# Kernel tuning notes

Hardware: AMD Instinct MI355X
Metric: run time of the kernel (lower is better)

The kernel has to match this reference:

```python
import jax, jax.numpy as jnp
import numpy as np

D_MODEL = 1024
NUM_HEADS = 16
SEQ_LEN = 2048
BATCH = 2
THETA = 10000.0


def apply_rope(x, positions, theta):
    # x: [..., seq, d_k]; positions: [seq]
    dk = x.shape[-1]
    half = dk // 2
    k = jnp.arange(half, dtype=jnp.float32)
    inv_freq = theta ** (-2.0 * k / dk)                 # [half]
    ang = positions.astype(jnp.float32)[:, None] * inv_freq  # [seq, half]
    cos, sin = jnp.cos(ang), jnp.sin(ang)
    xe = x[..., 0::2]   # even members of adjacent pairs
    xo = x[..., 1::2]
    out_e = cos * xe - sin * xo
    out_o = sin * xe + cos * xo
    # interleave pairs back: [..., seq, half, 2] -> [..., seq, dk]
    return jnp.stack([out_e, out_o], axis=-1).reshape(x.shape)


def setup_inputs() -> dict:
    key = jax.random.key(0)
    kx, kq, kk, kv, ko = jax.random.split(key, 5)
    sig = 1.0 / np.sqrt(D_MODEL)
    def tn(k):
        return jnp.clip(jax.random.normal(k, (D_MODEL, D_MODEL), jnp.float32), -3.0, 3.0) * sig
    return {
        "x": jax.random.normal(kx, (BATCH, SEQ_LEN, D_MODEL), jnp.float32),
        "q_proj_weight": tn(kq),
        "k_proj_weight": tn(kk),
        "v_proj_weight": tn(kv),
        "o_proj_weight": tn(ko),
        "token_positions": jnp.arange(SEQ_LEN, dtype=jnp.int32),
    }


def reference(x, q_proj_weight, k_proj_weight, v_proj_weight, o_proj_weight, token_positions):
    h = NUM_HEADS
    d = x.shape[-1]
    dh = d // h
    seq = x.shape[-2]
    Wq = q_proj_weight.reshape(h, dh, d)
    Wk = k_proj_weight.reshape(h, dh, d)
    Wv = v_proj_weight.reshape(h, dh, d)
    Q = jnp.einsum('bsd,hed->bhse', x, Wq)
    K = jnp.einsum('bsd,hed->bhse', x, Wk)
    V = jnp.einsum('bsd,hed->bhse', x, Wv)
    Q = apply_rope(Q, token_positions, THETA)
    K = apply_rope(K, token_positions, THETA)
    scores = jnp.einsum('bhqe,bhke->bhqk', Q, K) / jnp.sqrt(jnp.float32(dh))
    mask = jnp.tril(jnp.ones((seq, seq), dtype=bool))
    scores = jnp.where(mask, scores, -jnp.inf)
    probs = jax.nn.softmax(scores, axis=-1)
    att = jnp.einsum('bhqk,bhke->bhqe', probs, V)       # [b, h, s, dh]
    att = att.transpose(0, 2, 1, 3).reshape(x.shape[0], seq, d)  # concat heads
    return jnp.einsum('bsh,dh->bsd', att, o_proj_weight)
```

## Files before the change

### kernel.cpp

```cpp
#include <hip/hip_runtime.h>
#include <hip/hip_bf16.h>
#include <cstdint>
#include <cstddef>

#define DEV static __device__ __forceinline__

typedef __bf16 bf16x8 __attribute__((ext_vector_type(8)));
typedef float f32x4 __attribute__((ext_vector_type(4)));
typedef unsigned short u16;

static constexpr int BATCH = 2, SEQ = 2048, DM = 1024, NH = 16, DH = 64;
static constexpr int Kdim = 1024;
static constexpr int BS = BATCH * SEQ;

DEV u16 f2b(float f) {
  uint32_t u = __builtin_bit_cast(uint32_t, f);
  u += 0x7FFFu + ((u >> 16) & 1u);
  return (u16)(u >> 16);
}

DEV void gload_lds16(const void* g, void* l) {
  __builtin_amdgcn_global_load_lds((const __attribute__((address_space(1))) void*)g,
                                   (__attribute__((address_space(3))) void*)l, 16, 0, 0);
}

DEV void plswap32(uint32_t& a, uint32_t& b) {
  asm("v_permlane32_swap_b32 %0, %1" : "+v"(a), "+v"(b));
}
DEV void plswap16(uint32_t& a, uint32_t& b) {
  asm("v_permlane16_swap_b32 %0, %1" : "+v"(a), "+v"(b));
}

__global__ __launch_bounds__(256) void cast_all(const float* __restrict__ x,
    const float* __restrict__ wq, const float* __restrict__ wk,
    const float* __restrict__ wv, const float* __restrict__ wo,
    const int* __restrict__ pos,
    u16* __restrict__ xb, u16* __restrict__ wqb, u16* __restrict__ wkb,
    u16* __restrict__ wvb, u16* __restrict__ wob, float2* __restrict__ tab) {
  const int NX = (BATCH * SEQ * DM) / 4;
  const int NW = (DM * DM) / 4;
  const int NT = SEQ * 32;
  int i = blockIdx.x * blockDim.x + threadIdx.x;
  const int stride = gridDim.x * blockDim.x;
  for (; i < NX + 4 * NW + NT; i += stride) {
    if (i < NX + 4 * NW) {
      const float* src; u16* dst; int off;
      if (i < NX) { src = x; dst = xb; off = i; }
      else {
        const int j = i - NX, seg = j >> 18;
        off = j & (NW - 1);
        src = seg == 0 ? wq : seg == 1 ? wk : seg == 2 ? wv : wo;
        dst = seg == 0 ? wqb : seg == 1 ? wkb : seg == 2 ? wvb : wob;
      }
      float4 v = ((const float4*)src)[off];
      ushort4 o;
      o.x = f2b(v.x); o.y = f2b(v.y); o.z = f2b(v.z); o.w = f2b(v.w);
      ((ushort4*)dst)[off] = o;
    } else {
      const int t = i - NX - 4 * NW;
      const int s = t >> 5, j = t & 31;
      const float ang = (float)pos[s] * exp2f((float)j * -0.4152410118609203f);
      float sn, cs;
      sincosf(ang, &sn, &cs);
      tab[t] = make_float2(cs, sn);
    }
  }
}

template <int BN, bool OUTF32, int ROPE>
DEV void gemm_core(const u16* __restrict__ A, const u16* __restrict__ Bm,
                   void* __restrict__ Cout, int ldC, int m0, int n0,
                   u16* __restrict__ As, u16* __restrict__ Bs,
                   const float2* __restrict__ tab) {
  const int tid = threadIdx.x;
  const int lane = tid & 63, wid = tid >> 6;
  const int wr = (wid >> 1) * 64, wc = (wid & 1) * (BN / 2);
  const int frow = lane & 15, fgrp = lane >> 4;
  constexpr int NF = BN / 32;
  constexpr int BSZ = BN * 32;
  constexpr int NK = Kdim / 32;
  f32x4 acc[4][NF] = {};

  const int c0 = tid, c1 = tid + 256;
  const int ra0 = c0 >> 2, sa0 = (c0 & 3) ^ ((ra0 >> 1) & 3);
  const int ra1 = c1 >> 2, sa1 = (c1 & 3) ^ ((ra1 >> 1) & 3);
  const size_t gA0 = (size_t)(m0 + ra0) * Kdim + sa0 * 8;
  const size_t gA1 = (size_t)(m0 + ra1) * Kdim + sa1 * 8;
  const size_t gB0 = (size_t)(n0 + ra0) * Kdim + sa0 * 8;
  const size_t gB1 = (size_t)(n0 + ra1) * Kdim + sa1 * 8;

#define GSTAGE(bufi, kofs)                                                      \
  do {                                                                          \
    gload_lds16(A + gA0 + (kofs), As + (bufi) * 4096 + wid * 512);              \
    gload_lds16(A + gA1 + (kofs), As + (bufi) * 4096 + wid * 512 + 2048);       \
    gload_lds16(Bm + gB0 + (kofs), Bs + (bufi) * BSZ + wid * 512);              \
    if (BN == 128)                                                              \
      gload_lds16(Bm + gB1 + (kofs), Bs + (bufi) * BSZ + wid * 512 + 2048);     \
  } while (0)

  GSTAGE(0, 0);
  for (int kt = 0; kt < NK; ++kt) {
    const int buf = kt & 1;
    if (kt + 1 < NK) {
      GSTAGE((kt + 1) & 1, (kt + 1) * 32);
      if (BN == 128) asm volatile("s_waitcnt vmcnt(4)" ::: "memory");
      else           asm volatile("s_waitcnt vmcnt(3)" ::: "memory");
    } else {
      asm volatile("s_waitcnt vmcnt(0)" ::: "memory");
    }
    __builtin_amdgcn_s_barrier();

    bf16x8 af[4], bfr[NF];
#pragma unroll
    for (int i = 0; i < 4; ++i) {
      const int ra = wr + i * 16 + frow;
      af[i] = *(const bf16x8*)((const char*)(As + buf * 4096) + ra * 64 +
                               ((fgrp ^ ((ra >> 1) & 3)) * 16));
    }
#pragma unroll
    for (int f = 0; f < NF; ++f) {
      const int rb = wc + f * 16 + frow;
      bfr[f] = *(const bf16x8*)((const char*)(Bs + buf * BSZ) + rb * 64 +
                                ((fgrp ^ ((rb >> 1) & 3)) * 16));
    }
#pragma unroll
    for (int mi = 0; mi < 4; ++mi)
#pragma unroll
      for (int f = 0; f < NF; ++f)
        acc[mi][f] = __builtin_amdgcn_mfma_f32_16x16x32_bf16(af[mi], bfr[f], acc[mi][f], 0, 0, 0);

    __builtin_amdgcn_s_barrier();
  }
#undef GSTAGE

  const int colb = n0 + wc + frow;
  const int rowb = m0 + wr + fgrp * 4;
  if (ROPE) {
#pragma unroll
    for (int mi = 0; mi < 4; ++mi)
#pragma unroll
      for (int f = 0; f < NF; ++f) {
        const int col = colb + f * 16;
        const int j = (col & 63) >> 1;
#pragma unroll
        for (int r = 0; r < 4; ++r) {
          const float v = acc[mi][f][r];
          const float partner = __shfl_xor(v, 1);
          const int row = rowb + mi * 16 + r;
          const float2 cs_ = tab[(row & (SEQ - 1)) * 32 + j];
          float outv = (col & 1) ? fmaf(cs_.y, partner, cs_.x * v)
                                 : fmaf(cs_.x, v, -cs_.y * partner);
          if (ROPE == 1) outv *= 0.18033688011112043f;
          acc[mi][f][r] = outv;
        }
      }
  }
#pragma unroll
  for (int mi = 0; mi < 4; ++mi)
#pragma unroll
    for (int f = 0; f < NF; ++f)
#pragma unroll
      for (int r = 0; r < 4; ++r) {
        const int row = rowb + mi * 16 + r;
        const int col = colb + f * 16;
        const float v = acc[mi][f][r];
        if (OUTF32) ((float*)Cout)[(size_t)row * ldC + col] = v;
        else        ((u16*)Cout)[(size_t)row * ldC + col] = f2b(v);
      }
}

__global__ __launch_bounds__(256) void gemm_qkvt(const u16* __restrict__ xb,
    const u16* __restrict__ wq, const u16* __restrict__ wk, const u16* __restrict__ wv,
    u16* __restrict__ Qb, u16* __restrict__ Kb, u16* __restrict__ Vtb,
    const float2* __restrict__ tab) {
  __shared__ u16 As[2][4096], Bs[2][2048];
  const int f = blockIdx.x, z = blockIdx.z;
  const int xcd = f & 7, j = f >> 3;
  if (z == 0) {
    const int m0 = (xcd * 4 + (j >> 4)) * 128, n0 = (j & 15) * 64;
    gemm_core<64, false, 1>(xb, wq, Qb, DM, m0, n0, &As[0][0], &Bs[0][0], tab);
  } else if (z == 1) {
    const int m0 = (xcd * 4 + (j >> 4)) * 128, n0 = (j & 15) * 64;
    gemm_core<64, false, 2>(xb, wk, Kb, DM, m0, n0, &As[0][0], &Bs[0][0], tab);
  } else {
    const int m0 = xcd * 128, n0 = j * 64;
    gemm_core<64, false, 0>(wv, xb, Vtb, BS, m0, n0, &As[0][0], &Bs[0][0], nullptr);
  }
}

__global__ __launch_bounds__(256) void gemm_o(const u16* __restrict__ attb,
                                              const u16* __restrict__ wob,
                                              float* __restrict__ out) {
  __shared__ u16 As[2][4096], Bs[2][2048];
  const int f = blockIdx.x;
  const int xcd = f & 7, k = f >> 3;
  const int grp = xcd * 8 + (k >> 3);
  const int m0 = (grp >> 1) * 128;
  const int n0 = ((grp & 1) * 8 + (k & 7)) * 64;
  gemm_core<64, true, 0>(attb, wob, out, DM, m0, n0, &As[0][0], &Bs[0][0], nullptr);
}

__global__ __launch_bounds__(512, 4) void attn_kernel(const u16* __restrict__ Qb,
                                                      const u16* __restrict__ Kb,
                                                      const u16* __restrict__ Vtb,
                                                      u16* __restrict__ attb) {
  __shared__ __align__(16) unsigned char SM[73728];
  float* Of = (float*)SM;
  float* Ld = (float*)(SM + 65536);

  const int tid = threadIdx.x, lane = tid & 63, wid = tid >> 6;
  const int qh = wid >> 2, kq = wid & 3;
  const int flat = (int)blockIdx.x + 16 * (int)blockIdx.y;
  const int orig = (flat & 7) * 64 + (flat >> 3);
  const int xq = orig & 15;
  const int bh = orig >> 4;
  const int b = bh >> 4, h = bh & 15;
  const size_t base_bh = ((size_t)b * SEQ) * DM + h * DH;
  const int frow = lane & 15, fgrp = lane >> 4;
  const int kq32 = kq * 32;
  const int swz = (frow & 7) << 4;

  const u16* Ksrcs[2];
  const u16* Vsrcs[2];
#pragma unroll
  for (int i = 0; i < 2; ++i) {
    const int c = tid + i * 512;
    const int rk = c >> 3, s8 = (c & 7) ^ (rk & 7);
    Ksrcs[i] = Kb + base_bh + (size_t)rk * DM + s8 * 8;
    const int rv = c >> 4, s16 = (c & 15) ^ (rv & 7);
    Vsrcs[i] = Vtb + (size_t)(h * DH + rv) * BS + (size_t)b * SEQ + s16 * 8;
  }
  const int rq = tid >> 3, sq = (tid & 7) ^ (rq & 7);

#pragma unroll 1
  for (int phase = 0; phase < 2; ++phase) {
    const int qt = phase ? xq : 31 - xq;
    const int q0 = qt * 64;
    const int nkv = (qt >> 1) + 1;

    gload_lds16(Qb + base_bh + (size_t)(q0 + rq) * DM + sq * 8, (char*)SM + 65536 + tid * 16);
#pragma unroll
    for (int i = 0; i < 2; ++i) {
      gload_lds16(Ksrcs[i], (char*)SM + i * 8192 + tid * 16);
      gload_lds16(Vsrcs[i], (char*)SM + 32768 + i * 8192 + tid * 16);
    }
    __syncthreads();

    bf16x8 qf[2][2];
#pragma unroll
    for (int qs = 0; qs < 2; ++qs)
#pragma unroll
      for (int ks = 0; ks < 2; ++ks) {
        const int byte = ((qh * 32 + qs * 16 + frow) * 128 + ks * 64 + fgrp * 16) ^ swz;
        qf[qs][ks] = *(const bf16x8*)((const char*)SM + 65536 + byte);
      }

    f32x4 accO[2][4] = {};
    float l_lane[2] = {0.f, 0.f};

    for (int kt = 0; kt < nkv; ++kt) {
      const char* Kc = (const char*)SM + (kt & 1) * 16384;
      const char* Vc = (const char*)SM + 32768 + (kt & 1) * 16384;
      if (kt + 1 < nkv) {
        const size_t kvn = (size_t)(kt + 1) * 128;
        const int nb = (kt + 1) & 1;
#pragma unroll
        for (int i = 0; i < 2; ++i) {
          gload_lds16(Ksrcs[i] + kvn * DM, (char*)SM + nb * 16384 + i * 8192 + tid * 16);
          gload_lds16(Vsrcs[i] + kvn, (char*)SM + 32768 + nb * 16384 + i * 8192 + tid * 16);
        }
      }

      f32x4 sc[2][2] = {};
      __builtin_amdgcn_s_setprio(1);
#pragma unroll
      for (int tc = 0; tc < 2; ++tc)
#pragma unroll
        for (int ks = 0; ks < 2; ++ks) {
          const int byte = ((kq32 + tc * 16 + frow) * 128 + ks * 64 + fgrp * 16) ^ swz;
          const bf16x8 kf = *(const bf16x8*)(Kc + byte);
#pragma unroll
          for (int qs = 0; qs < 2; ++qs)
            sc[qs][tc] = __builtin_amdgcn_mfma_f32_16x16x32_bf16(kf, qf[qs][ks], sc[qs][tc], 0, 0, 0);
        }
      __builtin_amdgcn_s_setprio(0);

      if (kt == nkv - 1) {
        const int kv0 = kt * 128;
#pragma unroll
        for (int qs = 0; qs < 2; ++qs)
#pragma unroll
          for (int tc = 0; tc < 2; ++tc)
#pragma unroll
            for (int r = 0; r < 4; ++r)
              if (kv0 + kq32 + tc * 16 + fgrp * 4 + r > q0 + qh * 32 + qs * 16 + frow)
                sc[qs][tc][r] = -1e30f;
      }

      bf16x8 pf[2];
#pragma unroll
      for (int qs = 0; qs < 2; ++qs) {
        const float p00 = exp2f(sc[qs][0][0]), p01 = exp2f(sc[qs][0][1]);
        const float p02 = exp2f(sc[qs][0][2]), p03 = exp2f(sc[qs][0][3]);
        const float p10 = exp2f(sc[qs][1][0]), p11 = exp2f(sc[qs][1][1]);
        const float p12 = exp2f(sc[qs][1][2]), p13 = exp2f(sc[qs][1][3]);
        l_lane[qs] += ((p00 + p01) + (p02 + p03)) + ((p10 + p11) + (p12 + p13));
        union { __bf16 bb[2]; uint32_t uu; } c00, c01, c10, c11;
        c00.bb[0] = (__bf16)p00; c00.bb[1] = (__bf16)p01;
        c01.bb[0] = (__bf16)p02; c01.bb[1] = (__bf16)p03;
        c10.bb[0] = (__bf16)p10; c10.bb[1] = (__bf16)p11;
        c11.bb[0] = (__bf16)p12; c11.bb[1] = (__bf16)p13;
        uint32_t a0 = c00.uu, a1 = c01.uu, b0 = c10.uu, b1 = c11.uu;
        plswap32(a0, b0); plswap16(a0, b0);
        plswap32(a1, b1); plswap16(a1, b1);
        union { uint32_t w[4]; bf16x8 v; } pk;
        pk.w[0] = a0; pk.w[1] = a1; pk.w[2] = b0; pk.w[3] = b1;
        pf[qs] = pk.v;
      }

      __builtin_amdgcn_s_setprio(1);
#pragma unroll
      for (int te = 0; te < 4; ++te) {
        const int byte = ((te * 16 + frow) * 256 + kq * 64 + fgrp * 16) ^ swz;
        const bf16x8 vf = *(const bf16x8*)(Vc + byte);
#pragma unroll
        for (int qs = 0; qs < 2; ++qs)
          accO[qs][te] = __builtin_amdgcn_mfma_f32_16x16x32_bf16(pf[qs], vf, accO[qs][te], 0, 0, 0);
      }
      __builtin_amdgcn_s_setprio(0);
      __syncthreads();
    }

    float* myOf = Of + wid * 2048;
#pragma unroll
    for (int qs = 0; qs < 2; ++qs)
#pragma unroll
      for (int te = 0; te < 4; ++te)
#pragma unroll
        for (int r = 0; r < 4; ++r)
          myOf[(qs * 16 + fgrp * 4 + r) * 64 + te * 16 + frow] = accO[qs][te][r];
#pragma unroll
    for (int qs = 0; qs < 2; ++qs) {
      l_lane[qs] += __shfl_xor(l_lane[qs], 16);
      l_lane[qs] += __shfl_xor(l_lane[qs], 32);
    }
    if (fgrp == 0) {
#pragma unroll
      for (int qs = 0; qs < 2; ++qs) Ld[wid * 32 + qs * 16 + frow] = l_lane[qs];
    }
    __syncthreads();

#pragma unroll
    for (int ii = 0; ii < 2; ++ii) {
      const int ql = wid * 8 + fgrp * 2 + ii;
      const int hh = ql >> 5, qlh = ql & 31;
      f32x4 s = {};
      float lq = 0.f;
#pragma unroll
      for (int j = 0; j < 4; ++j) {
        s += *(const f32x4*)(Of + (hh * 4 + j) * 2048 + qlh * 64 + frow * 4);
        lq += Ld[(hh * 4 + j) * 32 + qlh];
      }
      const float inv = 1.0f / lq;
      ushort4 o;
      o.x = f2b(s[0] * inv); o.y = f2b(s[1] * inv);
      o.z = f2b(s[2] * inv); o.w = f2b(s[3] * inv);
      *(ushort4*)(attb + base_bh + (size_t)(q0 + ql) * DM + frow * 4) = o;
    }
    __syncthreads();
  }
}

extern "C" void kernel_launch(void* const* d_in, const int* in_sizes, int n_in,
                              void* d_out, int out_size, void* d_ws, size_t ws_size,
                              hipStream_t stream) {
  const float* x  = (const float*)d_in[0];
  const float* wq = (const float*)d_in[1];
  const float* wk = (const float*)d_in[2];
  const float* wv = (const float*)d_in[3];
  const float* wo = (const float*)d_in[4];
  const int* pos  = (const int*)d_in[5];
  float* out = (float*)d_out;
  (void)in_sizes; (void)n_in; (void)out_size; (void)ws_size;

  char* ws = (char*)d_ws;
  const size_t MB = 1024 * 1024;
  u16* xb   = (u16*)(ws);
  u16* wqb  = (u16*)(ws + 8 * MB);
  u16* wkb  = (u16*)(ws + 10 * MB);
  u16* wvb  = (u16*)(ws + 12 * MB);
  u16* wob  = (u16*)(ws + 14 * MB);
  u16* Qb   = (u16*)(ws + 16 * MB);
  u16* Kb   = (u16*)(ws + 24 * MB);
  u16* Vtb  = (u16*)(ws + 32 * MB);
  u16* attb = (u16*)(ws + 40 * MB);
  float2* tab = (float2*)(ws + 40 * MB);

  cast_all<<<2048, 256, 0, stream>>>(x, wq, wk, wv, wo, pos, xb, wqb, wkb, wvb, wob, tab);
  gemm_qkvt<<<dim3(512, 1, 3), 256, 0, stream>>>(xb, wqb, wkb, wvb, Qb, Kb, Vtb, tab);
  attn_kernel<<<dim3(16, 32), 512, 0, stream>>>(Qb, Kb, Vtb, attb);
  gemm_o<<<512, 256, 0, stream>>>(attb, wob, out);
}
```

Baseline: 117.0 us.

## Fuse Q and K projection GEMMs to share x tile loads

```diff
diff --git a/kernel.cpp b/kernel.cpp
--- a/kernel.cpp
+++ b/kernel.cpp
@@ -67,19 +67,16 @@
   }
 }
 
-template <int BN, bool OUTF32, int ROPE>
-DEV void gemm_core(const u16* __restrict__ A, const u16* __restrict__ Bm,
-                   void* __restrict__ Cout, int ldC, int m0, int n0,
-                   u16* __restrict__ As, u16* __restrict__ Bs,
-                   const float2* __restrict__ tab) {
+template <bool OUTF32>
+DEV void gemm_core64(const u16* __restrict__ A, const u16* __restrict__ Bm,
+                     void* __restrict__ Cout, int ldC, int m0, int n0,
+                     u16* __restrict__ As, u16* __restrict__ Bs) {
   const int tid = threadIdx.x;
   const int lane = tid & 63, wid = tid >> 6;
-  const int wr = (wid >> 1) * 64, wc = (wid & 1) * (BN / 2);
+  const int wr = (wid >> 1) * 64, wc = (wid & 1) * 32;
   const int frow = lane & 15, fgrp = lane >> 4;
-  constexpr int NF = BN / 32;
-  constexpr int BSZ = BN * 32;
   constexpr int NK = Kdim / 32;
-  f32x4 acc[4][NF] = {};
+  f32x4 acc[4][2] = {};
 
   const int c0 = tid, c1 = tid + 256;
   const int ra0 = c0 >> 2, sa0 = (c0 & 3) ^ ((ra0 >> 1) & 3);
@@ -87,15 +84,12 @@
   const size_t gA0 = (size_t)(m0 + ra0) * Kdim + sa0 * 8;
   const size_t gA1 = (size_t)(m0 + ra1) * Kdim + sa1 * 8;
   const size_t gB0 = (size_t)(n0 + ra0) * Kdim + sa0 * 8;
-  const size_t gB1 = (size_t)(n0 + ra1) * Kdim + sa1 * 8;
 
 #define GSTAGE(bufi, kofs)                                                      \
   do {                                                                          \
     gload_lds16(A + gA0 + (kofs), As + (bufi) * 4096 + wid * 512);              \
     gload_lds16(A + gA1 + (kofs), As + (bufi) * 4096 + wid * 512 + 2048);       \
-    gload_lds16(Bm + gB0 + (kofs), Bs + (bufi) * BSZ + wid * 512);              \
-    if (BN == 128)                                                              \
-      gload_lds16(Bm + gB1 + (kofs), Bs + (bufi) * BSZ + wid * 512 + 2048);     \
+    gload_lds16(Bm + gB0 + (kofs), Bs + (bufi) * 2048 + wid * 512);             \
   } while (0)
 
   GSTAGE(0, 0);
@@ -103,14 +97,13 @@
     const int buf = kt & 1;
     if (kt + 1 < NK) {
       GSTAGE((kt + 1) & 1, (kt + 1) * 32);
-      if (BN == 128) asm volatile("s_waitcnt vmcnt(4)" ::: "memory");
-      else           asm volatile("s_waitcnt vmcnt(3)" ::: "memory");
+      asm volatile("s_waitcnt vmcnt(3)" ::: "memory");
     } else {
       asm volatile("s_waitcnt vmcnt(0)" ::: "memory");
     }
     __builtin_amdgcn_s_barrier();
 
-    bf16x8 af[4], bfr[NF];
+    bf16x8 af[4], bfr[2];
 #pragma unroll
     for (int i = 0; i < 4; ++i) {
       const int ra = wr + i * 16 + frow;
@@ -118,15 +111,15 @@
                                ((fgrp ^ ((ra >> 1) & 3)) * 16));
     }
 #pragma unroll
-    for (int f = 0; f < NF; ++f) {
+    for (int f = 0; f < 2; ++f) {
       const int rb = wc + f * 16 + frow;
-      bfr[f] = *(const bf16x8*)((const char*)(Bs + buf * BSZ) + rb * 64 +
+      bfr[f] = *(const bf16x8*)((const char*)(Bs + buf * 2048) + rb * 64 +
                                 ((fgrp ^ ((rb >> 1) & 3)) * 16));
     }
 #pragma unroll
     for (int mi = 0; mi < 4; ++mi)
 #pragma unroll
-      for (int f = 0; f < NF; ++f)
+      for (int f = 0; f < 2; ++f)
         acc[mi][f] = __builtin_amdgcn_mfma_f32_16x16x32_bf16(af[mi], bfr[f], acc[mi][f], 0, 0, 0);
 
     __builtin_amdgcn_s_barrier();
@@ -135,30 +128,10 @@
 
   const int colb = n0 + wc + frow;
   const int rowb = m0 + wr + fgrp * 4;
-  if (ROPE) {
-#pragma unroll
-    for (int mi = 0; mi < 4; ++mi)
-#pragma unroll
-      for (int f = 0; f < NF; ++f) {
-        const int col = colb + f * 16;
-        const int j = (col & 63) >> 1;
-#pragma unroll
-        for (int r = 0; r < 4; ++r) {
-          const float v = acc[mi][f][r];
-          const float partner = __shfl_xor(v, 1);
-          const int row = rowb + mi * 16 + r;
-          const float2 cs_ = tab[(row & (SEQ - 1)) * 32 + j];
-          float outv = (col & 1) ? fmaf(cs_.y, partner, cs_.x * v)
-                                 : fmaf(cs_.x, v, -cs_.y * partner);
-          if (ROPE == 1) outv *= 0.18033688011112043f;
-          acc[mi][f][r] = outv;
-        }
-      }
-  }
 #pragma unroll
   for (int mi = 0; mi < 4; ++mi)
 #pragma unroll
-    for (int f = 0; f < NF; ++f)
+    for (int f = 0; f < 2; ++f)
 #pragma unroll
       for (int r = 0; r < 4; ++r) {
         const int row = rowb + mi * 16 + r;
@@ -169,23 +142,107 @@
       }
 }
 
-__global__ __launch_bounds__(256) void gemm_qkvt(const u16* __restrict__ xb,
-    const u16* __restrict__ wq, const u16* __restrict__ wk, const u16* __restrict__ wv,
-    u16* __restrict__ Qb, u16* __restrict__ Kb, u16* __restrict__ Vtb,
-    const float2* __restrict__ tab) {
+__global__ __launch_bounds__(256) void gemm_qk_fused(const u16* __restrict__ xb,
+    const u16* __restrict__ wq, const u16* __restrict__ wk,
+    u16* __restrict__ Qb, u16* __restrict__ Kb, const float2* __restrict__ tab) {
+  __shared__ u16 As[2][4096], Bq[2][2048], Bk[2][2048];
+  const int f = blockIdx.x;
+  const int xcd = f & 7, j = f >> 3;
+  const int m0 = (xcd * 4 + (j >> 4)) * 128, n0 = (j & 15) * 64;
+
+  const int tid = threadIdx.x;
+  const int lane = tid & 63, wid = tid >> 6;
+  const int wr = (wid >> 1) * 64, wc = (wid & 1) * 32;
+  const int frow = lane & 15, fgrp = lane >> 4;
+  constexpr int NK = Kdim / 32;
+  f32x4 accQ[4][2] = {}, accK[4][2] = {};
+
+  const int c0 = tid, c1 = tid + 256;
+  const int ra0 = c0 >> 2, sa0 = (c0 & 3) ^ ((ra0 >> 1) & 3);
+  const int ra1 = c1 >> 2, sa1 = (c1 & 3) ^ ((ra1 >> 1) & 3);
+  const size_t gA0 = (size_t)(m0 + ra0) * Kdim + sa0 * 8;
+  const size_t gA1 = (size_t)(m0 + ra1) * Kdim + sa1 * 8;
+  const size_t gB0 = (size_t)(n0 + ra0) * Kdim + sa0 * 8;
+
+#define QKSTAGE(bufi, kofs)                                                     \
+  do {                                                                          \
+    gload_lds16(xb + gA0 + (kofs), &As[bufi][0] + wid * 512);                   \
+    gload_lds16(xb + gA1 + (kofs), &As[bufi][0] + wid * 512 + 2048);            \
+    gload_lds16(wq + gB0 + (kofs), &Bq[bufi][0] + wid * 512);                   \
+    gload_lds16(wk + gB0 + (kofs), &Bk[bufi][0] + wid * 512);                   \
+  } while (0)
+
+  QKSTAGE(0, 0);
+  for (int kt = 0; kt < NK; ++kt) {
+    const int buf = kt & 1;
+    if (kt + 1 < NK) {
+      QKSTAGE((kt + 1) & 1, (kt + 1) * 32);
+      asm volatile("s_waitcnt vmcnt(4)" ::: "memory");
+    } else {
+      asm volatile("s_waitcnt vmcnt(0)" ::: "memory");
+    }
+    __builtin_amdgcn_s_barrier();
+
+    bf16x8 af[4], bq[2], bk[2];
+#pragma unroll
+    for (int i = 0; i < 4; ++i) {
+      const int ra = wr + i * 16 + frow;
+      af[i] = *(const bf16x8*)((const char*)&As[buf][0] + ra * 64 +
+                               ((fgrp ^ ((ra >> 1) & 3)) * 16));
+    }
+#pragma unroll
+    for (int f2 = 0; f2 < 2; ++f2) {
+      const int rb = wc + f2 * 16 + frow;
+      const int off = rb * 64 + ((fgrp ^ ((rb >> 1) & 3)) * 16);
+      bq[f2] = *(const bf16x8*)((const char*)&Bq[buf][0] + off);
+      bk[f2] = *(const bf16x8*)((const char*)&Bk[buf][0] + off);
+    }
+#pragma unroll
+    for (int mi = 0; mi < 4; ++mi)
+#pragma unroll
+      for (int f2 = 0; f2 < 2; ++f2) {
+        accQ[mi][f2] = __builtin_amdgcn_mfma_f32_16x16x32_bf16(af[mi], bq[f2], accQ[mi][f2], 0, 0, 0);
+        accK[mi][f2] = __builtin_amdgcn_mfma_f32_16x16x32_bf16(af[mi], bk[f2], accK[mi][f2], 0, 0, 0);
+      }
+
+    __builtin_amdgcn_s_barrier();
+  }
+#undef QKSTAGE
+
+  const int colb = n0 + wc + frow;
+  const int rowb = m0 + wr + fgrp * 4;
+#pragma unroll
+  for (int mi = 0; mi < 4; ++mi)
+#pragma unroll
+    for (int f2 = 0; f2 < 2; ++f2) {
+      const int col = colb + f2 * 16;
+      const int jj = (col & 63) >> 1;
+      const int odd = col & 1;
+#pragma unroll
+      for (int r = 0; r < 4; ++r) {
+        const int row = rowb + mi * 16 + r;
+        const float2 cs_ = tab[(row & (SEQ - 1)) * 32 + jj];
+        const float qv = accQ[mi][f2][r];
+        const float qp = __shfl_xor(qv, 1);
+        const float kv = accK[mi][f2][r];
+        const float kp = __shfl_xor(kv, 1);
+        float oq = odd ? fmaf(cs_.y, qp, cs_.x * qv) : fmaf(cs_.x, qv, -cs_.y * qp);
+        float ok = odd ? fmaf(cs_.y, kp, cs_.x * kv) : fmaf(cs_.x, kv, -cs_.y * kp);
+        oq *= 0.18033688011112043f;
+        Qb[(size_t)row * DM + col] = f2b(oq);
+        Kb[(size_t)row * DM + col] = f2b(ok);
+      }
+    }
+}
+
+__global__ __launch_bounds__(256) void gemm_vt(const u16* __restrict__ wv,
+                                               const u16* __restrict__ xb,
+                                               u16* __restrict__ Vtb) {
   __shared__ u16 As[2][4096], Bs[2][2048];
-  const int f = blockIdx.x, z = blockIdx.z;
+  const int f = blockIdx.x;
   const int xcd = f & 7, j = f >> 3;
-  if (z == 0) {
-    const int m0 = (xcd * 4 + (j >> 4)) * 128, n0 = (j & 15) * 64;
-    gemm_core<64, false, 1>(xb, wq, Qb, DM, m0, n0, &As[0][0], &Bs[0][0], tab);
-  } else if (z == 1) {
-    const int m0 = (xcd * 4 + (j >> 4)) * 128, n0 = (j & 15) * 64;
-    gemm_core<64, false, 2>(xb, wk, Kb, DM, m0, n0, &As[0][0], &Bs[0][0], tab);
-  } else {
-    const int m0 = xcd * 128, n0 = j * 64;
-    gemm_core<64, false, 0>(wv, xb, Vtb, BS, m0, n0, &As[0][0], &Bs[0][0], nullptr);
-  }
+  const int m0 = xcd * 128, n0 = j * 64;
+  gemm_core64<false>(wv, xb, Vtb, BS, m0, n0, &As[0][0], &Bs[0][0]);
 }
 
 __global__ __launch_bounds__(256) void gemm_o(const u16* __restrict__ attb,
@@ -197,7 +254,7 @@
   const int grp = xcd * 8 + (k >> 3);
   const int m0 = (grp >> 1) * 128;
   const int n0 = ((grp & 1) * 8 + (k & 7)) * 64;
-  gemm_core<64, true, 0>(attb, wob, out, DM, m0, n0, &As[0][0], &Bs[0][0], nullptr);
+  gemm_core64<true>(attb, wob, out, DM, m0, n0, &As[0][0], &Bs[0][0]);
 }
 
 __global__ __launch_bounds__(512, 4) void attn_kernel(const u16* __restrict__ Qb,
@@ -397,7 +454,8 @@
   float2* tab = (float2*)(ws + 40 * MB);
 
   cast_all<<<2048, 256, 0, stream>>>(x, wq, wk, wv, wo, pos, xb, wqb, wkb, wvb, wob, tab);
-  gemm_qkvt<<<dim3(512, 1, 3), 256, 0, stream>>>(xb, wqb, wkb, wvb, Qb, Kb, Vtb, tab);
+  gemm_qk_fused<<<512, 256, 0, stream>>>(xb, wqb, wkb, Qb, Kb, tab);
+  gemm_vt<<<512, 256, 0, stream>>>(wvb, xb, Vtb);
   attn_kernel<<<dim3(16, 32), 512, 0, stream>>>(Qb, Kb, Vtb, attb);
   gemm_o<<<512, 256, 0, stream>>>(attb, wob, out);
 }
```

Measured after the change: 118.4 us. Within noise of the previous version (+1.2%).
